# Performance work log

Hardware: AMD Instinct MI355X
Metric: run time of the kernel (lower is better)

## Reference

```python
import jax, jax.numpy as jnp
import numpy as np

B, C, H, W = 4, 2048, 32, 32


def conv1x1(x, Wt, b):
    # 1x1 conv == per-pixel matmul over channels
    return jnp.einsum('oc,bchw->bohw', Wt, x) + b[None, :, None, None]


def cross_attention(Q, K, V):
    b, c, h, w = Q.shape
    q = Q.reshape(b, c, h * w)   # [B, C, N]
    k = K.reshape(b, c, h * w)
    v = V.reshape(b, c, h * w)
    scores = jnp.einsum('bcn,bcm->bnm', q, k) / jnp.sqrt(jnp.asarray(c, jnp.float32))
    attn = jax.nn.softmax(scores, axis=-1)          # [B, N, N]
    out = jnp.einsum('bcm,bnm->bcn', v, attn)       # V @ attn^T
    return out.reshape(b, c, h, w)


def setup_inputs() -> dict:
    key = jax.random.key(0)
    ks = jax.random.split(key, 14)
    d = {
        'F_rgb': jax.random.normal(ks[0], (B, C, H, W), jnp.float32),
        'F_indices': jax.random.normal(ks[1], (B, C, H, W), jnp.float32),
    }
    names = ['q_rgb', 'k_rgb', 'v_rgb', 'q_ind', 'k_ind', 'v_ind']
    for i, n in enumerate(names):
        d['W_' + n] = jax.random.normal(ks[2 + 2 * i], (C, C), jnp.float32) * 0.02
        d['b_' + n] = jax.random.normal(ks[3 + 2 * i], (C,), jnp.float32) * 0.01
    return d


def reference(F_rgb, F_indices, W_q_rgb, b_q_rgb, W_k_rgb, b_k_rgb, W_v_rgb, b_v_rgb,
              W_q_ind, b_q_ind, W_k_ind, b_k_ind, W_v_ind, b_v_ind):
    # RGB queries attend over index features
    Q_rgb = conv1x1(F_rgb, W_q_rgb, b_q_rgb)
    K_ind = conv1x1(F_indices, W_k_ind, b_k_ind)
    V_ind = conv1x1(F_indices, W_v_ind, b_v_ind)
    F_rgb_attended = cross_attention(Q_rgb, K_ind, V_ind)
    # Index queries attend over RGB features
    Q_ind = conv1x1(F_indices, W_q_ind, b_q_ind)
    K_rgb = conv1x1(F_rgb, W_k_rgb, b_k_rgb)
    V_rgb = conv1x1(F_rgb, W_v_rgb, b_v_rgb)
    F_ind_attended = cross_attention(Q_ind, K_rgb, V_rgb)
    F_final = F_rgb_attended + F_ind_attended
    attention_weights = jnp.stack([F_rgb_attended, F_ind_attended], axis=1)  # [B,2,C,H,W]
    # pre_attention_outputs is an identity passthrough of the inputs
    return (F_final, F_rgb, F_indices, attention_weights)
```

## Files before the change

### kernel.cpp

```cpp
#include <hip/hip_runtime.h>

typedef __bf16 bf16x8 __attribute__((ext_vector_type(8)));
typedef float  f32x4  __attribute__((ext_vector_type(4)));
typedef unsigned short u16;

__device__ __forceinline__ u16 f2bf(float f) {
  unsigned u = __builtin_bit_cast(unsigned, f);
  u += 0x7fffu + ((u >> 16) & 1u);
  return (u16)(u >> 16);
}

using gvoid = __attribute__((address_space(1))) void;
using svoid = __attribute__((address_space(3))) void;
__device__ __forceinline__ void load_lds16(const void* g, void* s) {
  __builtin_amdgcn_global_load_lds((const gvoid*)g, (svoid*)s, 16, 0, 0);
}

__global__ void transpose_cvt(const float* __restrict__ F, u16* __restrict__ FT) {
  __shared__ float tile[32][33];
  const int b = blockIdx.z;
  const int n0 = blockIdx.x * 32, c0 = blockIdx.y * 32;
  const float* Fb = F + (long)b * 2048 * 1024;
  u16* FTb = FT + (long)b * 1024 * 2048;
  const int tx = threadIdx.x, ty = threadIdx.y;
#pragma unroll
  for (int i = 0; i < 4; ++i)
    tile[ty + i * 8][tx] = Fb[(long)(c0 + ty + i * 8) * 1024 + n0 + tx];
  __syncthreads();
#pragma unroll
  for (int i = 0; i < 4; ++i)
    FTb[(long)(n0 + ty + i * 8) * 2048 + c0 + tx] = f2bf(tile[tx][ty + i * 8]);
}

__global__ void cvt_bf16(const float* __restrict__ in, u16* __restrict__ out, int n4) {
  int i = blockIdx.x * 256 + threadIdx.x;
  if (i < n4) {
    float4 v = ((const float4*)in)[i];
    ushort4 o;
    o.x = f2bf(v.x); o.y = f2bf(v.y); o.z = f2bf(v.z); o.w = f2bf(v.w);
    ((ushort4*)out)[i] = o;
  }
}


#define BAR_ do { asm volatile("" ::: "memory"); __builtin_amdgcn_s_barrier(); \
                  asm volatile("" ::: "memory"); } while (0)
#define VMW asm volatile("s_waitcnt vmcnt(4)" ::: "memory")

#define STG(Mp, ld, row0, kt, off)                                                 \
  do {                                                                             \
    load_lds16(Mp + (long)((row0) + w * 8 + srow) * (ld) + (kt) * 64 + scol,       \
               sm + (off) + w * 1024);                                             \
    load_lds16(Mp + (long)((row0) + 64 + w * 8 + srow) * (ld) + (kt) * 64 + scol,  \
               sm + (off) + 8192 + w * 1024);                                      \
  } while (0)

#define RDA(off)                                                                   \
  _Pragma("unroll") for (int fm = 0; fm < 4; ++fm)                                 \
  _Pragma("unroll") for (int ks = 0; ks < 2; ++ks)                                 \
    fa[fm][ks] = *(const bf16x8*)(sm + (off) + aoff[fm] + kin[ks]);

#define RDB(off, dst)                                                              \
  _Pragma("unroll") for (int fn = 0; fn < 2; ++fn)                                 \
  _Pragma("unroll") for (int ks = 0; ks < 2; ++ks)                                 \
    dst[fn][ks] = *(const bf16x8*)(sm + (off) + boff[fn] + kin[ks]);

#define MMQ(qa, qb, fb)                                                            \
  __builtin_amdgcn_s_setprio(1);                                                   \
  _Pragma("unroll") for (int fm = 0; fm < 4; ++fm)                                 \
  _Pragma("unroll") for (int fn = 0; fn < 2; ++fn)                                 \
  _Pragma("unroll") for (int ks = 0; ks < 2; ++ks)                                 \
    acc[qa][qb][fm][fn] = __builtin_amdgcn_mfma_f32_16x16x32_bf16(                 \
        fa[fm][ks], fb[fn][ks], acc[qa][qb][fm][fn], 0, 0, 0);                     \
  __builtin_amdgcn_s_setprio(0);

template <int OUT_BF16, int BIAS_MODE>
__global__ __launch_bounds__(512, 2) void gemm256(
    const u16* __restrict__ A0p, const u16* __restrict__ B0p, void* __restrict__ D0p,
    const float* __restrict__ ba0, const float* __restrict__ bb0,
    const u16* __restrict__ A1p, const u16* __restrict__ B1p, void* __restrict__ D1p,
    const float* __restrict__ ba1, const float* __restrict__ bb1,
    int zsplit, int K, int lda, int ldb, int ldd,
    long sA, long sB, long sD) {
  __shared__ __attribute__((aligned(128))) char sm[131072];
  const int zb = blockIdx.z;
  const bool s1 = (zb >= zsplit);
  const int zz = s1 ? zb - zsplit : zb;
  const u16* Ag = (s1 ? A1p : A0p) + (long)zz * sA;
  const u16* Bg = (s1 ? B1p : B0p) + (long)zz * sB;
  char* Dg = (char*)(s1 ? D1p : D0p) + (long)zz * sD * (OUT_BF16 ? 2 : 4);
  const float* ba = s1 ? ba1 : ba0;
  const float* bb = s1 ? bb1 : bb0;
  const int m0 = blockIdx.y * 256, n0 = blockIdx.x * 256;
  const int t = threadIdx.x, w = t >> 6, l = t & 63;
  const int wr = w >> 2, wc = w & 3;
  const int lm = l & 15, lk = l >> 4;
  const int swz = (l & 7) << 4;
  const int srow = l >> 3;
  const int scol = ((l & 7) ^ srow) << 3;
  int aoff[4], boff[2], kin[2];
#pragma unroll
  for (int fm = 0; fm < 4; ++fm) aoff[fm] = (wr * 64 + fm * 16 + lm) * 128;
#pragma unroll
  for (int fn = 0; fn < 2; ++fn) boff[fn] = (wc * 32 + fn * 16 + lm) * 128;
  kin[0] = (lk * 16) ^ swz;
  kin[1] = (64 + lk * 16) ^ swz;

  f32x4 acc[2][2][4][2] = {};
  bf16x8 fa[4][2], fb0[2][2], fb1[2][2];

  const int nt = K >> 6;

  STG(Ag, lda, m0,       0, 0);
  STG(Bg, ldb, n0,       0, 32768);
  STG(Ag, lda, m0 + 128, 0, 16384);
  STG(Bg, ldb, n0 + 128, 0, 49152);
  STG(Ag, lda, m0,       1, 65536);
  STG(Bg, ldb, n0,       1, 65536 + 32768);
  VMW;
  BAR_;

  for (int u = 0; u < nt; u += 2) {
    const int t2 = (u + 2 < nt) ? u + 2 : nt - 1;
    const int t3 = (u + 3 < nt) ? u + 3 : nt - 1;
    RDA(0); RDB(32768, fb0);
    STG(Ag, lda, m0 + 128, u + 1, 65536 + 16384);
    BAR_; MMQ(0, 0, fb0); BAR_;
    RDB(49152, fb1);
    STG(Bg, ldb, n0 + 128, u + 1, 65536 + 49152);
    BAR_; MMQ(0, 1, fb1); BAR_;
    RDA(16384);
    STG(Ag, lda, m0, t2, 0);
    BAR_; MMQ(1, 0, fb0); BAR_;
    STG(Bg, ldb, n0, t2, 32768);
    BAR_; MMQ(1, 1, fb1); VMW; BAR_;
    RDA(65536); RDB(65536 + 32768, fb0);
    STG(Ag, lda, m0 + 128, t2, 16384);
    BAR_; MMQ(0, 0, fb0); BAR_;
    RDB(65536 + 49152, fb1);
    STG(Bg, ldb, n0 + 128, t2, 49152);
    BAR_; MMQ(0, 1, fb1); BAR_;
    RDA(65536 + 16384);
    STG(Ag, lda, m0, t3, 65536);
    BAR_; MMQ(1, 0, fb0); BAR_;
    STG(Bg, ldb, n0, t3, 65536 + 32768);
    BAR_; MMQ(1, 1, fb1); VMW; BAR_;
  }

#pragma unroll
  for (int qa = 0; qa < 2; ++qa)
#pragma unroll
    for (int qb = 0; qb < 2; ++qb)
#pragma unroll
      for (int fm = 0; fm < 4; ++fm)
#pragma unroll
        for (int fn = 0; fn < 2; ++fn) {
          const int row0 = m0 + qa * 128 + wr * 64 + fm * 16 + lk * 4;
          const int col  = n0 + qb * 128 + wc * 32 + fn * 16 + lm;
          float cb = 0.f;
          if (BIAS_MODE == 1) cb = (col < 2048) ? ba[col] : bb[col - 2048];
          f32x4 v = acc[qa][qb][fm][fn];
#pragma unroll
          for (int j = 0; j < 4; ++j) {
            float x = v[j] + cb;
            if (BIAS_MODE == 2) x += ba[row0 + j];
            const long idx = (long)(row0 + j) * ldd + col;
            if (OUT_BF16) ((u16*)Dg)[idx] = f2bf(x);
            else          ((float*)Dg)[idx] = x;
          }
        }
}

__global__ void softmax_rows(const float* __restrict__ S, u16* __restrict__ P,
                             float alpha) {
  const long row = blockIdx.x;
  const int t = threadIdx.x, l = t & 63, w = t >> 6;
  float4 v = ((const float4*)(S + row * 1024))[t];
  __shared__ float red[8];
  float m = fmaxf(fmaxf(v.x, v.y), fmaxf(v.z, v.w));
#pragma unroll
  for (int off = 32; off; off >>= 1) m = fmaxf(m, __shfl_xor(m, off));
  if (l == 0) red[w] = m;
  __syncthreads();
  m = fmaxf(fmaxf(red[0], red[1]), fmaxf(red[2], red[3]));
  float e0 = __expf((v.x - m) * alpha);
  float e1 = __expf((v.y - m) * alpha);
  float e2 = __expf((v.z - m) * alpha);
  float e3 = __expf((v.w - m) * alpha);
  float s = e0 + e1 + e2 + e3;
#pragma unroll
  for (int off = 32; off; off >>= 1) s += __shfl_xor(s, off);
  if (l == 0) red[4 + w] = s;
  __syncthreads();
  s = red[4] + red[5] + red[6] + red[7];
  const float inv = 1.0f / s;
  ushort4 o;
  o.x = f2bf(e0 * inv); o.y = f2bf(e1 * inv);
  o.z = f2bf(e2 * inv); o.w = f2bf(e3 * inv);
  ((ushort4*)(P + row * 1024))[t] = o;
}

__global__ void final_add(const float4* __restrict__ aw, float4* __restrict__ dst) {
  const long i = (long)blockIdx.x * 256 + threadIdx.x;
  const long b = i >> 19;
  const long r = i & 524287;
  float4 a = aw[b * 1048576 + r];
  float4 c = aw[b * 1048576 + 524288 + r];
  float4 o;
  o.x = a.x + c.x; o.y = a.y + c.y; o.z = a.z + c.z; o.w = a.w + c.w;
  dst[i] = o;
}

extern "C" void kernel_launch(void* const* d_in, const int* in_sizes, int n_in,
                              void* d_out, int out_size, void* d_ws, size_t ws_size,
                              hipStream_t stream) {
  (void)in_sizes; (void)n_in; (void)out_size; (void)ws_size;
  const float* F_rgb = (const float*)d_in[0];
  const float* F_ind = (const float*)d_in[1];
  const float* bq_rgb = (const float*)d_in[3];
  const float* bk_rgb = (const float*)d_in[5];
  const float* bv_rgb = (const float*)d_in[7];
  const float* bq_ind = (const float*)d_in[9];
  const float* bk_ind = (const float*)d_in[11];
  const float* bv_ind = (const float*)d_in[13];

  char* ws = (char*)d_ws;
  u16* FT_rgb  = (u16*)(ws);
  u16* FT_ind  = (u16*)(ws + 16777216);
  u16* Wqk_rgb = (u16*)(ws + 33554432);
  u16* Wqk_ind = (u16*)(ws + 50331648);
  u16* Wv_rgb  = (u16*)(ws + 67108864);
  u16* Wv_ind  = (u16*)(ws + 75497472);
  u16* QKT_rgb = (u16*)(ws + 83886080);
  u16* QKT_ind = (u16*)(ws + 117440512);
  u16* V_rgb   = (u16*)(ws + 150994944);
  u16* V_ind   = (u16*)(ws + 167772160);
  float* S     = (float*)(ws + 184549376);
  u16*   P     = (u16*)(ws + 218103808);

  float* out       = (float*)d_out;
  float* out_final = out;
  float* out_Frgb  = out + 8388608;
  float* out_Find  = out + 16777216;
  float* AW        = out + 25165824;

  transpose_cvt<<<dim3(32, 64, 4), dim3(32, 8), 0, stream>>>(F_rgb, FT_rgb);
  transpose_cvt<<<dim3(32, 64, 4), dim3(32, 8), 0, stream>>>(F_ind, FT_ind);
  cvt_bf16<<<4096, 256, 0, stream>>>((const float*)d_in[2],  Wqk_rgb,           1048576);
  cvt_bf16<<<4096, 256, 0, stream>>>((const float*)d_in[4],  Wqk_rgb + 4194304, 1048576);
  cvt_bf16<<<4096, 256, 0, stream>>>((const float*)d_in[8],  Wqk_ind,           1048576);
  cvt_bf16<<<4096, 256, 0, stream>>>((const float*)d_in[10], Wqk_ind + 4194304, 1048576);
  cvt_bf16<<<4096, 256, 0, stream>>>((const float*)d_in[6],  Wv_rgb,            1048576);
  cvt_bf16<<<4096, 256, 0, stream>>>((const float*)d_in[12], Wv_ind,            1048576);

  gemm256<1, 1><<<dim3(16, 4, 4), 512, 0, stream>>>(
      FT_rgb, Wqk_rgb, QKT_rgb, bq_rgb, bk_rgb,
      FT_rgb, Wqk_rgb, QKT_rgb, bq_rgb, bk_rgb,
      8, 2048, 2048, 2048, 4096, 2097152L, 0L, 4194304L);
  gemm256<1, 1><<<dim3(16, 4, 4), 512, 0, stream>>>(
      FT_ind, Wqk_ind, QKT_ind, bq_ind, bk_ind,
      FT_ind, Wqk_ind, QKT_ind, bq_ind, bk_ind,
      8, 2048, 2048, 2048, 4096, 2097152L, 0L, 4194304L);

  gemm256<1, 2><<<dim3(4, 8, 8), 512, 0, stream>>>(
      Wv_rgb, FT_rgb, V_rgb, bv_rgb, bv_rgb,
      Wv_ind, FT_ind, V_ind, bv_ind, bv_ind,
      4, 2048, 2048, 2048, 1024, 0L, 2097152L, 2097152L);

  gemm256<0, 0><<<dim3(4, 4, 8), 512, 0, stream>>>(
      QKT_rgb, QKT_ind + 2048, S, nullptr, nullptr,
      QKT_ind, QKT_rgb + 2048, S + 4194304, nullptr, nullptr,
      4, 2048, 4096, 4096, 1024, 4194304L, 4194304L, 1048576L);

  softmax_rows<<<8192, 256, 0, stream>>>(S, P, 0.02209708691207961f);

  gemm256<0, 0><<<dim3(4, 8, 8), 512, 0, stream>>>(
      V_ind, P, AW, nullptr, nullptr,
      V_rgb, P + 4194304, AW + 2097152, nullptr, nullptr,
      4, 1024, 1024, 1024, 1024, 2097152L, 1048576L, 4194304L);

  final_add<<<8192, 256, 0, stream>>>((const float4*)AW, (float4*)out_final);
  hipMemcpyAsync(out_Frgb, F_rgb, 33554432, hipMemcpyDeviceToDevice, stream);
  hipMemcpyAsync(out_Find, F_ind, 33554432, hipMemcpyDeviceToDevice, stream);
}
```

Before: 394.5 us.

## Merge launches, split-K scores GEMM with atomics, fuse final add into PV epilogue

New measurement: 448.3 us. +13.6%, slower.

```diff
diff --git a/kernel.cpp b/kernel.cpp
--- a/kernel.cpp
+++ b/kernel.cpp
@@ -16,9 +16,19 @@
   __builtin_amdgcn_global_load_lds((const gvoid*)g, (svoid*)s, 16, 0, 0);
 }
 
-__global__ void transpose_cvt(const float* __restrict__ F, u16* __restrict__ FT) {
+__global__ void zero4(float4* __restrict__ S4, float4* __restrict__ F4) {
+  const int i = blockIdx.x * 256 + threadIdx.x;
+  const float4 z = {0.f, 0.f, 0.f, 0.f};
+  if (i < 2097152) S4[i] = z;
+  else             F4[i - 2097152] = z;
+}
+
+__global__ void transpose_cvt(const float* __restrict__ Fr, const float* __restrict__ Fi,
+                              u16* __restrict__ FTr, u16* __restrict__ FTi) {
   __shared__ float tile[32][33];
-  const int b = blockIdx.z;
+  const int b = blockIdx.z & 3;
+  const float* F = (blockIdx.z >= 4) ? Fi : Fr;
+  u16* FT = (blockIdx.z >= 4) ? FTi : FTr;
   const int n0 = blockIdx.x * 32, c0 = blockIdx.y * 32;
   const float* Fb = F + (long)b * 2048 * 1024;
   u16* FTb = FT + (long)b * 1024 * 2048;
@@ -32,14 +42,22 @@
     FTb[(long)(n0 + ty + i * 8) * 2048 + c0 + tx] = f2bf(tile[tx][ty + i * 8]);
 }
 
-__global__ void cvt_bf16(const float* __restrict__ in, u16* __restrict__ out, int n4) {
-  int i = blockIdx.x * 256 + threadIdx.x;
-  if (i < n4) {
-    float4 v = ((const float4*)in)[i];
-    ushort4 o;
-    o.x = f2bf(v.x); o.y = f2bf(v.y); o.z = f2bf(v.z); o.w = f2bf(v.w);
-    ((ushort4*)out)[i] = o;
+__global__ void cvt6(const float* __restrict__ s0, const float* __restrict__ s1,
+                     const float* __restrict__ s2, const float* __restrict__ s3,
+                     const float* __restrict__ s4, const float* __restrict__ s5,
+                     u16* __restrict__ dst) {
+  const int blk = blockIdx.x;
+  const int chunk = blk >> 12;
+  const int i = (blk & 4095) * 256 + threadIdx.x;
+  const float* src;
+  switch (chunk) {
+    case 0: src = s0; break; case 1: src = s1; break; case 2: src = s2; break;
+    case 3: src = s3; break; case 4: src = s4; break; default: src = s5; break;
   }
+  float4 v = ((const float4*)src)[i];
+  ushort4 o;
+  o.x = f2bf(v.x); o.y = f2bf(v.y); o.z = f2bf(v.z); o.w = f2bf(v.w);
+  ((ushort4*)(dst + (long)chunk * 4194304))[i] = o;
 }
 
 
@@ -74,23 +92,27 @@
         fa[fm][ks], fb[fn][ks], acc[qa][qb][fm][fn], 0, 0, 0);                     \
   __builtin_amdgcn_s_setprio(0);
 
-template <int OUT_BF16, int BIAS_MODE>
+template <int OUT_BF16, int BIAS_MODE, int EPI, int KSPLIT>
 __global__ __launch_bounds__(512, 2) void gemm256(
     const u16* __restrict__ A0p, const u16* __restrict__ B0p, void* __restrict__ D0p,
     const float* __restrict__ ba0, const float* __restrict__ bb0,
     const u16* __restrict__ A1p, const u16* __restrict__ B1p, void* __restrict__ D1p,
     const float* __restrict__ ba1, const float* __restrict__ bb1,
+    float* __restrict__ F0p, float* __restrict__ F1p, long sF,
     int zsplit, int K, int lda, int ldb, int ldd,
     long sA, long sB, long sD) {
   __shared__ __attribute__((aligned(128))) char sm[131072];
-  const int zb = blockIdx.z;
+  int zb = blockIdx.z;
+  int kh = 0;
+  if (KSPLIT) { kh = zb >> 3; zb &= 7; }
   const bool s1 = (zb >= zsplit);
   const int zz = s1 ? zb - zsplit : zb;
-  const u16* Ag = (s1 ? A1p : A0p) + (long)zz * sA;
-  const u16* Bg = (s1 ? B1p : B0p) + (long)zz * sB;
+  const u16* Ag = (s1 ? A1p : A0p) + (long)zz * sA + (long)kh * K;
+  const u16* Bg = (s1 ? B1p : B0p) + (long)zz * sB + (long)kh * K;
   char* Dg = (char*)(s1 ? D1p : D0p) + (long)zz * sD * (OUT_BF16 ? 2 : 4);
   const float* ba = s1 ? ba1 : ba0;
   const float* bb = s1 ? bb1 : bb0;
+  float* Fg = (EPI == 2) ? ((s1 ? F1p : F0p) + (long)zz * sF) : nullptr;
   const int m0 = blockIdx.y * 256, n0 = blockIdx.x * 256;
   const int t = threadIdx.x, w = t >> 6, l = t & 63;
   const int wr = w >> 2, wc = w & 3;
@@ -165,8 +187,13 @@
             float x = v[j] + cb;
             if (BIAS_MODE == 2) x += ba[row0 + j];
             const long idx = (long)(row0 + j) * ldd + col;
-            if (OUT_BF16) ((u16*)Dg)[idx] = f2bf(x);
-            else          ((float*)Dg)[idx] = x;
+            if (EPI == 1) {
+              unsafeAtomicAdd((float*)Dg + idx, x);
+            } else {
+              if (OUT_BF16) ((u16*)Dg)[idx] = f2bf(x);
+              else          ((float*)Dg)[idx] = x;
+              if (EPI == 2) unsafeAtomicAdd(Fg + idx, x);
+            }
           }
         }
 }
@@ -198,17 +225,6 @@
   o.x = f2bf(e0 * inv); o.y = f2bf(e1 * inv);
   o.z = f2bf(e2 * inv); o.w = f2bf(e3 * inv);
   ((ushort4*)(P + row * 1024))[t] = o;
-}
-
-__global__ void final_add(const float4* __restrict__ aw, float4* __restrict__ dst) {
-  const long i = (long)blockIdx.x * 256 + threadIdx.x;
-  const long b = i >> 19;
-  const long r = i & 524287;
-  float4 a = aw[b * 1048576 + r];
-  float4 c = aw[b * 1048576 + 524288 + r];
-  float4 o;
-  o.x = a.x + c.x; o.y = a.y + c.y; o.z = a.z + c.z; o.w = a.w + c.w;
-  dst[i] = o;
 }
 
 extern "C" void kernel_launch(void* const* d_in, const int* in_sizes, int n_in,
@@ -227,7 +243,8 @@
   char* ws = (char*)d_ws;
   u16* FT_rgb  = (u16*)(ws);
   u16* FT_ind  = (u16*)(ws + 16777216);
-  u16* Wqk_rgb = (u16*)(ws + 33554432);
+  u16* Wall    = (u16*)(ws + 33554432);
+  u16* Wqk_rgb = Wall;
   u16* Wqk_ind = (u16*)(ws + 50331648);
   u16* Wv_rgb  = (u16*)(ws + 67108864);
   u16* Wv_ind  = (u16*)(ws + 75497472);
@@ -244,42 +261,39 @@
   float* out_Find  = out + 16777216;
   float* AW        = out + 25165824;
 
-  transpose_cvt<<<dim3(32, 64, 4), dim3(32, 8), 0, stream>>>(F_rgb, FT_rgb);
-  transpose_cvt<<<dim3(32, 64, 4), dim3(32, 8), 0, stream>>>(F_ind, FT_ind);
-  cvt_bf16<<<4096, 256, 0, stream>>>((const float*)d_in[2],  Wqk_rgb,           1048576);
-  cvt_bf16<<<4096, 256, 0, stream>>>((const float*)d_in[4],  Wqk_rgb + 4194304, 1048576);
-  cvt_bf16<<<4096, 256, 0, stream>>>((const float*)d_in[8],  Wqk_ind,           1048576);
-  cvt_bf16<<<4096, 256, 0, stream>>>((const float*)d_in[10], Wqk_ind + 4194304, 1048576);
-  cvt_bf16<<<4096, 256, 0, stream>>>((const float*)d_in[6],  Wv_rgb,            1048576);
-  cvt_bf16<<<4096, 256, 0, stream>>>((const float*)d_in[12], Wv_ind,            1048576);
-
-  gemm256<1, 1><<<dim3(16, 4, 4), 512, 0, stream>>>(
+  zero4<<<16384, 256, 0, stream>>>((float4*)S, (float4*)out_final);
+
+  transpose_cvt<<<dim3(32, 64, 8), dim3(32, 8), 0, stream>>>(F_rgb, F_ind, FT_rgb, FT_ind);
+  cvt6<<<24576, 256, 0, stream>>>((const float*)d_in[2], (const float*)d_in[4],
+                                  (const float*)d_in[8], (const float*)d_in[10],
+                                  (const float*)d_in[6], (const float*)d_in[12], Wall);
+
+  gemm256<1, 1, 0, 0><<<dim3(16, 4, 8), 512, 0, stream>>>(
       FT_rgb, Wqk_rgb, QKT_rgb, bq_rgb, bk_rgb,
-      FT_rgb, Wqk_rgb, QKT_rgb, bq_rgb, bk_rgb,
-      8, 2048, 2048, 2048, 4096, 2097152L, 0L, 4194304L);
-  gemm256<1, 1><<<dim3(16, 4, 4), 512, 0, stream>>>(
       FT_ind, Wqk_ind, QKT_ind, bq_ind, bk_ind,
-      FT_ind, Wqk_ind, QKT_ind, bq_ind, bk_ind,
-      8, 2048, 2048, 2048, 4096, 2097152L, 0L, 4194304L);
-
-  gemm256<1, 2><<<dim3(4, 8, 8), 512, 0, stream>>>(
+      nullptr, nullptr, 0L,
+      4, 2048, 2048, 2048, 4096, 2097152L, 0L, 4194304L);
+
+  gemm256<1, 2, 0, 0><<<dim3(4, 8, 8), 512, 0, stream>>>(
       Wv_rgb, FT_rgb, V_rgb, bv_rgb, bv_rgb,
       Wv_ind, FT_ind, V_ind, bv_ind, bv_ind,
+      nullptr, nullptr, 0L,
       4, 2048, 2048, 2048, 1024, 0L, 2097152L, 2097152L);
 
-  gemm256<0, 0><<<dim3(4, 4, 8), 512, 0, stream>>>(
+  gemm256<0, 0, 1, 1><<<dim3(4, 4, 16), 512, 0, stream>>>(
       QKT_rgb, QKT_ind + 2048, S, nullptr, nullptr,
       QKT_ind, QKT_rgb + 2048, S + 4194304, nullptr, nullptr,
-      4, 2048, 4096, 4096, 1024, 4194304L, 4194304L, 1048576L);
+      nullptr, nullptr, 0L,
+      4, 1024, 4096, 4096, 1024, 4194304L, 4194304L, 1048576L);
 
   softmax_rows<<<8192, 256, 0, stream>>>(S, P, 0.02209708691207961f);
 
-  gemm256<0, 0><<<dim3(4, 8, 8), 512, 0, stream>>>(
+  gemm256<0, 0, 2, 0><<<dim3(4, 8, 8), 512, 0, stream>>>(
       V_ind, P, AW, nullptr, nullptr,
       V_rgb, P + 4194304, AW + 2097152, nullptr, nullptr,
+      out_final, out_final, 2097152L,
       4, 1024, 1024, 1024, 1024, 2097152L, 1048576L, 4194304L);
 
-  final_add<<<8192, 256, 0, stream>>>((const float4*)AW, (float4*)out_final);
   hipMemcpyAsync(out_Frgb, F_rgb, 33554432, hipMemcpyDeviceToDevice, stream);
   hipMemcpyAsync(out_Find, F_ind, 33554432, hipMemcpyDeviceToDevice, stream);
 }
```
